# Kernel tuning notes

Measured on AMD Instinct MI355X. Metric: run time of the kernel, lower is better.

The kernel has to match this reference:

```python
import jax, jax.numpy as jnp
import numpy as np

E = 1024
H = 16
D = E // H  # head dim 64
B = 2
S = 2048


def setup_inputs() -> dict:
    key = jax.random.key(0)
    k1, k2, k3, k4, k5 = jax.random.split(key, 5)
    scale = 1.0 / np.sqrt(E)
    return {
        "x": jax.random.normal(k1, (B, S, E), dtype=jnp.float32),
        "W_in": jax.random.normal(k2, (E, 3 * E), dtype=jnp.float32) * scale,
        "b_in": jnp.zeros((3 * E,), dtype=jnp.float32),
        "W_out": jax.random.normal(k3, (E, E), dtype=jnp.float32) * scale,
        "b_out": jnp.zeros((E,), dtype=jnp.float32),
        "causal_mask": 1,
    }


def reference(x, W_in, b_in, W_out, b_out, causal_mask):
    b, s, e = x.shape
    qkv = x @ W_in + b_in                      # [B,S,3E]
    q, k, v = jnp.split(qkv, 3, axis=-1)
    # [B,S,E] -> [B,H,S,D]
    q = q.reshape(b, s, H, D).transpose(0, 2, 1, 3)
    k = k.reshape(b, s, H, D).transpose(0, 2, 1, 3)
    v = v.reshape(b, s, H, D).transpose(0, 2, 1, 3)
    scores = jnp.einsum("bhqd,bhkd->bhqk", q, k)
    if causal_mask:
        # mask applied before scaling in the original; -inf is scale-invariant
        mask = jnp.triu(jnp.ones((s, s), dtype=bool), k=1)
        scores = jnp.where(mask, -jnp.inf, scores)
    scores = scores / np.sqrt(D)
    weight = jax.nn.softmax(scores, axis=-1)
    out = jnp.einsum("bhqk,bhkd->bhqd", weight, v)   # [B,H,S,D]
    out = out.transpose(0, 2, 1, 3).reshape(b, s, e)
    return out @ W_out + b_out
```

## Files before the change

### kernel.cpp

```cpp
#include <hip/hip_runtime.h>
#include <hip/hip_bf16.h>
#include <cmath>

typedef __bf16 bf16;
typedef __attribute__((ext_vector_type(8))) __bf16 bf16x8;
typedef __attribute__((ext_vector_type(4))) __bf16 bf16x4;
typedef __attribute__((ext_vector_type(4))) float f32x4;
typedef __attribute__((ext_vector_type(16))) float f32x16;
typedef unsigned int u32;

constexpr int S  = 2048;
constexpr int E  = 1024;
constexpr int H  = 16;
constexpr int D  = 64;
constexpr int B  = 2;
constexpr int M  = B * S;
constexpr int N3 = 3 * E;
constexpr int NROWS = B * H * S;

__constant__ int P_tab_d[16] = {1,1,1,1,1,2,2,2,2,2,2,3,3,3,3,3};
__constant__ int S_tab_d[16] = {0,1,2,3,4,5,7,9,11,13,15,17,20,23,26,29};
__constant__ int c_ord_d[32] = {15,15,10,10, 15,14,14,14,13,9,9,4,
                                13,13,12,12,8,8, 12,11,11,11,7,7,3,
                                6,6, 5,5,2, 1, 0};
__constant__ int p_ord_d[32] = {1,2,0,1, 0,0,1,2,2,0,1,0,
                                0,1,1,2,0,1, 0,0,1,2,0,1,0,
                                0,1, 0,1,0, 0, 0};

static __device__ __forceinline__ void gload16(const void* g, void* l) {
  __builtin_amdgcn_global_load_lds((const __attribute__((address_space(1))) void*)g,
                                   (__attribute__((address_space(3))) void*)l, 16, 0, 0);
}

static __device__ __forceinline__ u32 pack2(float a, float b) {
  union { bf16 h[2]; u32 u; } r;
  r.h[0] = (bf16)a; r.h[1] = (bf16)b;
  return r.u;
}
typedef union { u32 w[4]; bf16x8 v; } FU;

__global__ __launch_bounds__(256) void k_prep(
    const float* __restrict__ x, bf16* __restrict__ xb,
    const float* __restrict__ W_in, bf16* __restrict__ wtin,
    const float* __restrict__ W_out, bf16* __restrict__ wtout)
{
  const int bid = blockIdx.x;
  if (bid < 4096) {
    const int i = (bid * 256 + threadIdx.x) * 4;
    const float4 v = *(const float4*)(x + i);
    bf16x4 o = { (bf16)v.x, (bf16)v.y, (bf16)v.z, (bf16)v.w };
    *(bf16x4*)(xb + i) = o;
  } else {
    __shared__ float t[32][33];
    const float* in;
    bf16* out;
    int R, C, bx, by;
    if (bid < 4096 + 3072) {
      const int b = bid - 4096;
      in = W_in; out = wtin; R = E; C = N3;
      bx = b % (N3 / 32); by = b / (N3 / 32);
    } else {
      const int b = bid - 4096 - 3072;
      in = W_out; out = wtout; R = E; C = E;
      bx = b % (E / 32); by = b / (E / 32);
    }
    const int c0 = bx * 32, r0 = by * 32;
    const int tx = threadIdx.x & 31, ty = threadIdx.x >> 5;
    #pragma unroll
    for (int j = 0; j < 32; j += 8)
      t[ty + j][tx] = in[(size_t)(r0 + ty + j) * C + c0 + tx];
    __syncthreads();
    #pragma unroll
    for (int j = 0; j < 32; j += 8)
      out[(size_t)(c0 + ty + j) * R + r0 + tx] = (bf16)t[tx][ty + j];
  }
}

template<int EPI>
__global__ __launch_bounds__(256) void k_gemm(
    const bf16* __restrict__ A, const bf16* __restrict__ Bt,
    const float* __restrict__ bias, float* __restrict__ outF,
    bf16* __restrict__ oQ, bf16* __restrict__ oK, bf16* __restrict__ oV,
    int Kdim, int Nn)
{
  __shared__ __align__(16) char smem[65536];
  const int tid = threadIdx.x;
  const int lane = tid & 63, w = tid >> 6;
  const int lane15 = lane & 15, quad = lane >> 4;
  const int wm = w >> 1, wn = w & 1;

  const int nbx = Nn >> 7;
  const int nwg = gridDim.x;
  const int bid = blockIdx.x;
  const int swz = (bid & 7) * (nwg >> 3) + (bid >> 3);
  const int bn0 = (swz % nbx) * 128;
  const int bm0 = (swz / nbx) * 128;

  const int so0 = w * 1024 + lane * 16;
  int srow[4], slk[4];
  #pragma unroll
  for (int p = 0; p < 4; ++p) {
    const int o = p * 4096 + so0;
    const int row = o >> 7, cbyte = o & 127;
    srow[p] = row;
    slk[p] = (cbyte ^ ((row & 7) << 4)) >> 1;
  }

  f32x4 acc[4][4] = {};
  const int nkt = Kdim >> 6;

  #pragma unroll
  for (int p = 0; p < 4; ++p) {
    gload16(A  + (size_t)(bm0 + srow[p]) * Kdim + slk[p], smem +         p * 4096 + w * 1024);
    gload16(Bt + (size_t)(bn0 + srow[p]) * Kdim + slk[p], smem + 32768 + p * 4096 + w * 1024);
  }

  #pragma unroll 1
  for (int kt = 0; kt < nkt; ++kt) {
    const int cur = kt & 1;
    __builtin_amdgcn_s_barrier();
    if (kt + 1 < nkt) {
      const int k0 = (kt + 1) << 6;
      const int nb = (cur ^ 1) * 16384;
      #pragma unroll
      for (int p = 0; p < 4; ++p) {
        gload16(A  + (size_t)(bm0 + srow[p]) * Kdim + k0 + slk[p],
                smem + nb +         p * 4096 + w * 1024);
        gload16(Bt + (size_t)(bn0 + srow[p]) * Kdim + k0 + slk[p],
                smem + nb + 32768 + p * 4096 + w * 1024);
      }
      asm volatile("s_waitcnt vmcnt(8)" ::: "memory");
    } else {
      asm volatile("s_waitcnt vmcnt(0)" ::: "memory");
    }
    __builtin_amdgcn_s_barrier();

    const char* cA = smem + cur * 16384;
    const char* cB = smem + 32768 + cur * 16384;
    #pragma unroll
    for (int kk = 0; kk < 2; ++kk) {
      bf16x8 af[4], bfr[4];
      #pragma unroll
      for (int f = 0; f < 4; ++f) {
        const int ra = wm * 64 + f * 16 + lane15;
        af[f] = *(const bf16x8*)(cA + ra * 128 +
                 ((kk * 64 + (quad << 4)) ^ ((ra & 7) << 4)));
        const int rb = wn * 64 + f * 16 + lane15;
        bfr[f] = *(const bf16x8*)(cB + rb * 128 +
                 ((kk * 64 + (quad << 4)) ^ ((rb & 7) << 4)));
      }
      #pragma unroll
      for (int i = 0; i < 4; ++i)
        #pragma unroll
        for (int j = 0; j < 4; ++j)
          acc[i][j] = __builtin_amdgcn_mfma_f32_16x16x32_bf16(af[i], bfr[j], acc[i][j], 0, 0, 0);
    }
  }

  if constexpr (EPI == 1) {
    #pragma unroll
    for (int i = 0; i < 4; ++i)
      #pragma unroll
      for (int j = 0; j < 4; ++j) {
        const int n = bn0 + wn * 64 + j * 16 + lane15;
        const float bv = bias[n];
        #pragma unroll
        for (int r = 0; r < 4; ++r) {
          const int m = bm0 + wm * 64 + i * 16 + quad * 4 + r;
          outF[(size_t)m * E + n] = acc[i][j][r] + bv;
        }
      }
  } else {
    const int which = bn0 >> 10;
    const int b  = bm0 >> 11;
    const int s0 = bm0 & (S - 1);
    const int cn0 = bn0 & (E - 1);
    if (which < 2) {
      __builtin_amdgcn_s_barrier();
      char* lC = smem;
      #pragma unroll
      for (int j = 0; j < 4; ++j) {
        const int n_loc = wn * 64 + j * 16 + lane15;
        const float bv = bias[bn0 + n_loc];
        #pragma unroll
        for (int i = 0; i < 4; ++i)
          #pragma unroll
          for (int r = 0; r < 4; ++r) {
            const int m_loc = wm * 64 + i * 16 + quad * 4 + r;
            *(bf16*)(lC + m_loc * 256 + ((n_loc * 2) ^ ((m_loc & 7) << 4))) =
                (bf16)(acc[i][j][r] + bv);
          }
      }
      __builtin_amdgcn_s_barrier();
      const int h0 = cn0 >> 6;
      #pragma unroll
      for (int it = 0; it < 8; ++it) {
        const int cch = w * 64 + it * 8 + (lane >> 3);
        const int m_loc = cch >> 1, hh = cch & 1, piece = lane & 7;
        const bf16x8 vv = *(const bf16x8*)(lC + m_loc * 256 +
                          ((hh * 128 + piece * 16) ^ ((m_loc & 7) << 4)));
        if (which == 0) {
          *(bf16x8*)(oQ + ((size_t)(b * H + h0 + hh) * S + s0 + m_loc) * D + piece * 8) = vv;
        } else {
          const size_t hb = (size_t)(b * H + h0 + hh) * S * D;
          const int tile = (s0 + m_loc) >> 6;
          const int row = m_loc & 63;
          *(bf16x8*)(oK + hb + (size_t)tile * 4096 + (piece >> 1) * 1024 +
                     (row >> 5) * 512 + (32 * (piece & 1) + (row & 31)) * 8) = vv;
        }
      }
    } else {
      #pragma unroll
      for (int j = 0; j < 4; ++j) {
        const int n_loc = wn * 64 + j * 16 + lane15;
        const int cn = cn0 + n_loc;
        const int hv = cn >> 6, dd = cn & 63;
        const float bv = bias[bn0 + n_loc];
        const size_t hb = (size_t)(b * H + hv) * S * D;
        #pragma unroll
        for (int i = 0; i < 4; ++i) {
          const int scol_g = s0 + wm * 64 + i * 16 + quad * 4;
          const int vtile = scol_g >> 6;
          const int cg = (scol_g & 63) >> 3;
          bf16x4 pk = { (bf16)(acc[i][j][0] + bv), (bf16)(acc[i][j][1] + bv),
                        (bf16)(acc[i][j][2] + bv), (bf16)(acc[i][j][3] + bv) };
          *(bf16x4*)(oV + hb + (size_t)vtile * 4096 + (cg >> 1) * 1024 +
                     (dd >> 5) * 512 + (32 * (cg & 1) + (dd & 31)) * 8 +
                     (quad & 1) * 4) = pk;
        }
      }
    }
  }
}

__global__ __launch_bounds__(256, 4) void k_attn(
    const bf16* __restrict__ Qb, const bf16* __restrict__ Kf, const bf16* __restrict__ Vf,
    bf16* __restrict__ pO0, bf16* __restrict__ pO1,
    float* __restrict__ pM, float* __restrict__ pL, const int* __restrict__ cmask)
{
  __shared__ float corr_lds[4][32];
  __shared__ float lrow_lds[4][32];

  const int tid = threadIdx.x, lane = tid & 63, w = tid >> 6;
  const int h = lane >> 5, q31 = lane & 31;
  const int bh = blockIdx.x;
  const int yy = blockIdx.y;
  const int c  = c_ord_d[yy];
  const int p  = p_ord_d[yy];
  const int Pc = P_tab_d[c];
  const int sslot = S_tab_d[c] + p;
  const int causal = cmask[0];
  const float S2 = 0.18033688011112042f;

  const bf16* Qh = Qb + (size_t)bh * S * D;
  const bf16* Kh = Kf + (size_t)bh * S * D;
  const bf16* Vh = Vf + (size_t)bh * S * D;

  const int nt = causal ? (2 * c + 2) : (S / 64);
  const int t0 = (p * nt) / Pc;
  const int t1 = ((p + 1) * nt) / Pc;
  const int q0w = c * 128 + 32 * w;
  const int qg  = q0w + q31;
  const int t1w = causal ? min(t1, ((q0w + 31) >> 6) + 1) : t1;

  bf16x8 qf[4];
  #pragma unroll
  for (int ds = 0; ds < 4; ++ds)
    qf[ds] = *(const bf16x8*)(Qh + (size_t)qg * D + 16 * ds + 8 * h);

  f32x16 o0 = {}, o1 = {};
  float mrun = -INFINITY, lr = 0.f;

  #pragma unroll 1
  for (int t = t0; t < t1w; ++t) {
    const bf16* ktb = Kh + (size_t)t * 4096;
    const bf16* vtb = Vh + (size_t)t * 4096;

    bf16x8 kf0[4], kf1[4];
    #pragma unroll
    for (int ds = 0; ds < 4; ++ds) {
      kf0[ds] = *(const bf16x8*)(ktb + ds * 1024 +       lane * 8);
      kf1[ds] = *(const bf16x8*)(ktb + ds * 1024 + 512 + lane * 8);
    }

    f32x16 s0v = {}, s1v = {};
    __builtin_amdgcn_s_setprio(1);
    #pragma unroll
    for (int ds = 0; ds < 4; ++ds) {
      s0v = __builtin_amdgcn_mfma_f32_32x32x16_bf16(kf0[ds], qf[ds], s0v, 0, 0, 0);
      s1v = __builtin_amdgcn_mfma_f32_32x32x16_bf16(kf1[ds], qf[ds], s1v, 0, 0, 0);
    }
    __builtin_amdgcn_s_setprio(0);

    if (causal && (64 * t + 63 > q0w)) {
      #pragma unroll
      for (int rr = 0; rr < 16; ++rr) {
        const int kg = 64 * t + (rr & 3) + 8 * (rr >> 2) + 4 * h;
        if (kg > qg)      s0v[rr] = -INFINITY;
        if (kg + 32 > qg) s1v[rr] = -INFINITY;
      }
    }

    float a8[8];
    #pragma unroll
    for (int i = 0; i < 8; ++i)
      a8[i] = fmaxf(fmaxf(s0v[i], s0v[i + 8]), fmaxf(s1v[i], s1v[i + 8]));
    float tmax = fmaxf(fmaxf(fmaxf(a8[0], a8[1]), fmaxf(a8[2], a8[3])),
                       fmaxf(fmaxf(a8[4], a8[5]), fmaxf(a8[6], a8[7])));
    tmax = fmaxf(tmax, __shfl_xor(tmax, 32, 64));

    const bool nogrow = __all(tmax <= mrun);
    const float mnew = nogrow ? mrun : fmaxf(mrun, tmax);
    float corrf = 1.f;
    if (!nogrow) {
      corrf = __builtin_amdgcn_exp2f((mrun - mnew) * S2);
      corr_lds[w][q31] = corrf;
    }
    const float msc = mnew * S2;

    #pragma unroll
    for (int rr = 0; rr < 16; ++rr) {
      s0v[rr] = __builtin_amdgcn_exp2f(__builtin_fmaf(s0v[rr], S2, -msc));
      s1v[rr] = __builtin_amdgcn_exp2f(__builtin_fmaf(s1v[rr], S2, -msc));
    }

    float b8[8];
    #pragma unroll
    for (int i = 0; i < 8; ++i)
      b8[i] = (s0v[i] + s0v[i + 8]) + (s1v[i] + s1v[i + 8]);
    float psum = ((b8[0] + b8[1]) + (b8[2] + b8[3])) + ((b8[4] + b8[5]) + (b8[6] + b8[7]));
    psum += __shfl_xor(psum, 32, 64);
    lr = lr * corrf + psum;
    mrun = mnew;

    u32 pk[8][2];
    #pragma unroll
    for (int jj = 0; jj < 4; ++jj) {
      pk[jj][0]     = pack2(s0v[4 * jj],     s0v[4 * jj + 1]);
      pk[jj][1]     = pack2(s0v[4 * jj + 2], s0v[4 * jj + 3]);
      pk[jj + 4][0] = pack2(s1v[4 * jj],     s1v[4 * jj + 1]);
      pk[jj + 4][1] = pack2(s1v[4 * jj + 2], s1v[4 * jj + 3]);
    }

    if (!nogrow) {
      #pragma unroll
      for (int j = 0; j < 4; ++j) {
        const f32x4 cv = *(const f32x4*)&corr_lds[w][8 * j + 4 * h];
        #pragma unroll
        for (int sr = 0; sr < 4; ++sr) {
          o0[4 * j + sr] *= cv[sr];
          o1[4 * j + sr] *= cv[sr];
        }
      }
    }

    __builtin_amdgcn_s_setprio(1);
    #pragma unroll
    for (int ks = 0; ks < 4; ++ks) {
      u32 a0 = pk[2 * ks][0], b0 = pk[2 * ks + 1][0];
      u32 a1 = pk[2 * ks][1], b1 = pk[2 * ks + 1][1];
      asm volatile("v_permlane32_swap_b32 %0, %1" : "+v"(a0), "+v"(b0));
      asm volatile("v_permlane32_swap_b32 %0, %1" : "+v"(a1), "+v"(b1));
      FU f; f.w[0] = a0; f.w[1] = a1; f.w[2] = b0; f.w[3] = b1;
      const bf16x8 vf0 = *(const bf16x8*)(vtb + ks * 1024 +       lane * 8);
      const bf16x8 vf1 = *(const bf16x8*)(vtb + ks * 1024 + 512 + lane * 8);
      o0 = __builtin_amdgcn_mfma_f32_32x32x16_bf16(f.v, vf0, o0, 0, 0, 0);
      o1 = __builtin_amdgcn_mfma_f32_32x32x16_bf16(f.v, vf1, o1, 0, 0, 0);
    }
    __builtin_amdgcn_s_setprio(0);
  }

  const int slotbase = ((bh & 15) * 32 + sslot) * 128;
  if (h == 0) {
    pM[(size_t)(bh * 32 + sslot) * 128 + 32 * w + q31] = mrun;
    pL[(size_t)(bh * 32 + sslot) * 128 + 32 * w + q31] = lr;
  }
  lrow_lds[w][q31] = lr;
  bf16* po = (bh < 16 ? pO0 : pO1) + (size_t)slotbase * D;
  #pragma unroll
  for (int j = 0; j < 4; ++j) {
    const f32x4 lv = *(const f32x4*)&lrow_lds[w][8 * j + 4 * h];
    #pragma unroll
    for (int sr = 0; sr < 4; ++sr) {
      const int rr = 4 * j + sr;
      const float inv = lv[sr] > 0.f ? 1.0f / lv[sr] : 0.f;
      const int qloc = 32 * w + (rr & 3) + 8 * (rr >> 2) + 4 * h;
      bf16* dst = po + (size_t)qloc * D;
      dst[q31]      = (bf16)(o0[rr] * inv);
      dst[32 + q31] = (bf16)(o1[rr] * inv);
    }
  }
}

__global__ __launch_bounds__(256) void k_combine(
    const bf16* __restrict__ pO0, const bf16* __restrict__ pO1,
    const float* __restrict__ pM, const float* __restrict__ pL,
    bf16* __restrict__ AO)
{
  const float S2 = 0.18033688011112042f;
  const int idx = blockIdx.x * 256 + threadIdx.x;
  const int row = idx >> 3, d0 = (idx & 7) * 8;
  const int bh = row >> 11, s = row & 2047;
  const int c = s >> 7, local = s & 127;
  const int Pc = P_tab_d[c], Sc = S_tab_d[c];
  const bf16* pbase = (bh < 16 ? pO0 : pO1);

  float mv[3], lv[3];
  float m = -INFINITY;
  #pragma unroll
  for (int p = 0; p < 3; ++p) {
    if (p < Pc) {
      mv[p] = pM[(size_t)(bh * 32 + Sc + p) * 128 + local];
      lv[p] = pL[(size_t)(bh * 32 + Sc + p) * 128 + local];
      m = fmaxf(m, mv[p]);
    }
  }
  float wsum = 0.f, wv[3];
  #pragma unroll
  for (int p = 0; p < 3; ++p) {
    wv[p] = 0.f;
    if (p < Pc && lv[p] > 0.f) {
      wv[p] = lv[p] * __builtin_amdgcn_exp2f((mv[p] - m) * S2);
      wsum += wv[p];
    }
  }
  const float inv = 1.0f / wsum;
  float acc[8] = {};
  #pragma unroll
  for (int p = 0; p < 3; ++p) {
    if (p < Pc) {
      const bf16x8 a = *(const bf16x8*)(pbase +
          ((size_t)((bh & 15) * 32 + Sc + p) * 128 + local) * D + d0);
      #pragma unroll
      for (int i = 0; i < 8; ++i)
        acc[i] += wv[p] * (float)a[i];
    }
  }
  bf16x8 o;
  #pragma unroll
  for (int i = 0; i < 8; ++i)
    o[i] = (bf16)(acc[i] * inv);
  const int bb = row >> 15, hh = (row >> 11) & 15;
  *(bf16x8*)(AO + ((size_t)(bb * S + s)) * E + hh * D + d0) = o;
}

extern "C" void kernel_launch(void* const* d_in, const int* in_sizes, int n_in,
                              void* d_out, int out_size, void* d_ws, size_t ws_size,
                              hipStream_t stream) {
  (void)in_sizes; (void)n_in; (void)out_size; (void)ws_size;
  const float* x     = (const float*)d_in[0];
  const float* W_in  = (const float*)d_in[1];
  const float* b_in  = (const float*)d_in[2];
  const float* W_out = (const float*)d_in[3];
  const float* b_out = (const float*)d_in[4];
  const int*   cmask = (const int*)d_in[5];

  char* ws = (char*)d_ws;
  bf16* xb    = (bf16*)ws; ws += (size_t)M * E * 2;
  bf16* wtin  = (bf16*)ws; ws += (size_t)N3 * E * 2;
  bf16* wtout = (bf16*)ws; ws += (size_t)E * E * 2;
  bf16* qB    = (bf16*)ws; ws += (size_t)B * H * S * D * 2;
  bf16* kF    = (bf16*)ws; ws += (size_t)B * H * S * D * 2;
  bf16* vF    = (bf16*)ws; ws += (size_t)B * H * S * D * 2;
  bf16* ao    = (bf16*)ws; ws += (size_t)M * E * 2;
  bf16* pO1   = (bf16*)ws; ws += (size_t)NROWS * D * 2;
  float* pMb  = (float*)ws; ws += (size_t)2 * NROWS * 4;
  float* pLb  = (float*)ws; ws += (size_t)2 * NROWS * 4;
  bf16* pO0   = xb;

  k_prep<<<4096 + 3072 + 1024, 256, 0, stream>>>(x, xb, W_in, wtin, W_out, wtout);
  k_gemm<0><<<dim3((M / 128) * (N3 / 128)), 256, 0, stream>>>(
      xb, wtin, b_in, nullptr, qB, kF, vF, E, N3);
  k_attn<<<dim3(32, 32), 256, 0, stream>>>(qB, kF, vF, pO0, pO1, pMb, pLb, cmask);
  k_combine<<<NROWS * 8 / 256, 256, 0, stream>>>(pO0, pO1, pMb, pLb, ao);
  k_gemm<1><<<dim3((M / 128) * (E / 128)), 256, 0, stream>>>(
      ao, wtout, b_out, (float*)d_out, nullptr, nullptr, nullptr, E, E);
}
```

Measured before the change: 106.0 us.

## Compute softmax row sums with an extra MFMA against ones

The per-tile row-sum reduction (VALU adds plus a cross-half shuffle) is replaced by a third MFMA per k-step that multiplies the bf16 probability fragment by a vector of ones, so the row sums arrive in the output-accumulator layout. This removes the LDS round trip for the final normalisation and lets the correction factor scale the sum accumulator the same way as the output. The row max now uses three-input max chains to cut VALU instruction count. The cost is 50% more MFMA work in the PV stage, 16 extra accumulator registers, and row sums taken from bf16-rounded probabilities instead of fp32 values.

```diff
diff --git a/kernel.cpp b/kernel.cpp
--- a/kernel.cpp
+++ b/kernel.cpp
@@ -38,6 +38,10 @@
   return r.u;
 }
 typedef union { u32 w[4]; bf16x8 v; } FU;
+
+static __device__ __forceinline__ float m3(float a, float b, float c) {
+  return fmaxf(fmaxf(a, b), c);
+}
 
 __global__ __launch_bounds__(256) void k_prep(
     const float* __restrict__ x, bf16* __restrict__ xb,
@@ -239,7 +243,6 @@
     float* __restrict__ pM, float* __restrict__ pL, const int* __restrict__ cmask)
 {
   __shared__ float corr_lds[4][32];
-  __shared__ float lrow_lds[4][32];
 
   const int tid = threadIdx.x, lane = tid & 63, w = tid >> 6;
   const int h = lane >> 5, q31 = lane & 31;
@@ -268,8 +271,12 @@
   for (int ds = 0; ds < 4; ++ds)
     qf[ds] = *(const bf16x8*)(Qh + (size_t)qg * D + 16 * ds + 8 * h);
 
-  f32x16 o0 = {}, o1 = {};
-  float mrun = -INFINITY, lr = 0.f;
+  bf16x8 ones;
+  #pragma unroll
+  for (int i = 0; i < 8; ++i) ones[i] = (bf16)1.0f;
+
+  f32x16 o0 = {}, o1 = {}, osum = {};
+  float mrun = -INFINITY;
 
   #pragma unroll 1
   for (int t = t0; t < t1w; ++t) {
@@ -301,20 +308,23 @@
       }
     }
 
-    float a8[8];
+    float t8[8];
     #pragma unroll
     for (int i = 0; i < 8; ++i)
-      a8[i] = fmaxf(fmaxf(s0v[i], s0v[i + 8]), fmaxf(s1v[i], s1v[i + 8]));
-    float tmax = fmaxf(fmaxf(fmaxf(a8[0], a8[1]), fmaxf(a8[2], a8[3])),
-                       fmaxf(fmaxf(a8[4], a8[5]), fmaxf(a8[6], a8[7])));
+      t8[i] = m3(s0v[i], s0v[i + 8], s1v[i]);
+    float v0 = m3(t8[0], t8[1], s1v[8]);
+    float v1 = m3(t8[2], t8[3], s1v[9]);
+    float v2 = m3(t8[4], t8[5], s1v[10]);
+    float v3 = m3(t8[6], t8[7], s1v[11]);
+    float w0 = m3(v0, v1, s1v[12]);
+    float w1 = m3(v2, v3, s1v[13]);
+    float tmax = fmaxf(m3(w0, w1, s1v[14]), s1v[15]);
     tmax = fmaxf(tmax, __shfl_xor(tmax, 32, 64));
 
     const bool nogrow = __all(tmax <= mrun);
     const float mnew = nogrow ? mrun : fmaxf(mrun, tmax);
-    float corrf = 1.f;
     if (!nogrow) {
-      corrf = __builtin_amdgcn_exp2f((mrun - mnew) * S2);
-      corr_lds[w][q31] = corrf;
+      corr_lds[w][q31] = __builtin_amdgcn_exp2f((mrun - mnew) * S2);
     }
     const float msc = mnew * S2;
 
@@ -323,14 +333,6 @@
       s0v[rr] = __builtin_amdgcn_exp2f(__builtin_fmaf(s0v[rr], S2, -msc));
       s1v[rr] = __builtin_amdgcn_exp2f(__builtin_fmaf(s1v[rr], S2, -msc));
     }
-
-    float b8[8];
-    #pragma unroll
-    for (int i = 0; i < 8; ++i)
-      b8[i] = (s0v[i] + s0v[i + 8]) + (s1v[i] + s1v[i + 8]);
-    float psum = ((b8[0] + b8[1]) + (b8[2] + b8[3])) + ((b8[4] + b8[5]) + (b8[6] + b8[7]));
-    psum += __shfl_xor(psum, 32, 64);
-    lr = lr * corrf + psum;
     mrun = mnew;
 
     u32 pk[8][2];
@@ -348,8 +350,9 @@
         const f32x4 cv = *(const f32x4*)&corr_lds[w][8 * j + 4 * h];
         #pragma unroll
         for (int sr = 0; sr < 4; ++sr) {
-          o0[4 * j + sr] *= cv[sr];
-          o1[4 * j + sr] *= cv[sr];
+          o0[4 * j + sr]   *= cv[sr];
+          o1[4 * j + sr]   *= cv[sr];
+          osum[4 * j + sr] *= cv[sr];
         }
       }
     }
@@ -364,8 +367,9 @@
       FU f; f.w[0] = a0; f.w[1] = a1; f.w[2] = b0; f.w[3] = b1;
       const bf16x8 vf0 = *(const bf16x8*)(vtb + ks * 1024 +       lane * 8);
       const bf16x8 vf1 = *(const bf16x8*)(vtb + ks * 1024 + 512 + lane * 8);
-      o0 = __builtin_amdgcn_mfma_f32_32x32x16_bf16(f.v, vf0, o0, 0, 0, 0);
-      o1 = __builtin_amdgcn_mfma_f32_32x32x16_bf16(f.v, vf1, o1, 0, 0, 0);
+      o0   = __builtin_amdgcn_mfma_f32_32x32x16_bf16(f.v, vf0, o0, 0, 0, 0);
+      o1   = __builtin_amdgcn_mfma_f32_32x32x16_bf16(f.v, vf1, o1, 0, 0, 0);
+      osum = __builtin_amdgcn_mfma_f32_32x32x16_bf16(f.v, ones, osum, 0, 0, 0);
     }
     __builtin_amdgcn_s_setprio(0);
   }
@@ -373,22 +377,21 @@
   const int slotbase = ((bh & 15) * 32 + sslot) * 128;
   if (h == 0) {
     pM[(size_t)(bh * 32 + sslot) * 128 + 32 * w + q31] = mrun;
-    pL[(size_t)(bh * 32 + sslot) * 128 + 32 * w + q31] = lr;
-  }
-  lrow_lds[w][q31] = lr;
+  }
+  if (q31 == 0) {
+    float* dst = pL + (size_t)(bh * 32 + sslot) * 128 + 32 * w;
+    #pragma unroll
+    for (int rr = 0; rr < 16; ++rr)
+      dst[(rr & 3) + 8 * (rr >> 2) + 4 * h] = osum[rr];
+  }
   bf16* po = (bh < 16 ? pO0 : pO1) + (size_t)slotbase * D;
   #pragma unroll
-  for (int j = 0; j < 4; ++j) {
-    const f32x4 lv = *(const f32x4*)&lrow_lds[w][8 * j + 4 * h];
-    #pragma unroll
-    for (int sr = 0; sr < 4; ++sr) {
-      const int rr = 4 * j + sr;
-      const float inv = lv[sr] > 0.f ? 1.0f / lv[sr] : 0.f;
-      const int qloc = 32 * w + (rr & 3) + 8 * (rr >> 2) + 4 * h;
-      bf16* dst = po + (size_t)qloc * D;
-      dst[q31]      = (bf16)(o0[rr] * inv);
-      dst[32 + q31] = (bf16)(o1[rr] * inv);
-    }
+  for (int rr = 0; rr < 16; ++rr) {
+    const float inv = osum[rr] > 0.f ? 1.0f / osum[rr] : 0.f;
+    const int qloc = 32 * w + (rr & 3) + 8 * (rr >> 2) + 4 * h;
+    bf16* dst = po + (size_t)qloc * D;
+    dst[q31]      = (bf16)(o0[rr] * inv);
+    dst[32 + q31] = (bf16)(o1[rr] * inv);
   }
 }
 
```

Measured after the change: 107.6 us. No clear change (+1.5%).
